# Optimization experiments

Measured on AMD Instinct MI355X. Metric: run time of the kernel, lower is better.

## Reference

```python
import jax, jax.numpy as jnp
import numpy as np

B, N, DEG = 8, 8192, 16
E = B * N * DEG
K1 = 2458  # ceil(0.3*8192)
K2 = 738   # ceil(0.3*2458)
NUM_CLASSES = 10


def gat(x, src, dst, emask, W, a_s, a_d, bias):
    # PyG GATConv with add_self_loops=True, negative_slope=0.2, concat heads
    n = x.shape[0]
    H, F = a_s.shape
    xp = (x @ W).reshape(n, H, F)                      # [n,H,F]
    al_s = (xp * a_s).sum(-1)                          # [n,H]
    al_d = (xp * a_d).sum(-1)
    loops = jnp.arange(n, dtype=src.dtype)
    s2 = jnp.concatenate([src, loops])
    d2 = jnp.concatenate([dst, loops])
    m2 = jnp.concatenate([emask, jnp.ones(n, bool)])
    e = jax.nn.leaky_relu(al_s[s2] + al_d[d2], 0.2)    # [E+n,H]
    e = jnp.where(m2[:, None], e, -1e9)
    emax = jax.ops.segment_max(e, d2, num_segments=n)
    ex = jnp.where(m2[:, None], jnp.exp(e - emax[d2]), 0.0)
    den = jax.ops.segment_sum(ex, d2, num_segments=n)
    msg = ex[:, :, None] * xp[s2]                      # [E+n,H,F]
    out = jax.ops.segment_sum(msg, d2, num_segments=n) / den[:, :, None]
    return out.reshape(n, H * F) + bias


def inorm(x):
    # PyG InstanceNorm (affine=False): per-graph per-channel normalization
    xb = x.reshape(B, -1, x.shape[-1])
    mu = xb.mean(1, keepdims=True)
    var = ((xb - mu) ** 2).mean(1, keepdims=True)
    return ((xb - mu) / jnp.sqrt(var + 1e-5)).reshape(x.shape)


def topk_pool(x, src, dst, emask, p, k):
    # TopKPooling: score = tanh(x.p/|p|), keep top-k per graph, scale x by score
    n_tot = x.shape[0]
    n = n_tot // B
    score = jnp.tanh((x @ p) / jnp.linalg.norm(p))
    sv, si = jax.lax.top_k(score.reshape(B, n), k)     # [B,k]
    xg = jnp.take_along_axis(x.reshape(B, n, -1), si[:, :, None], axis=1)
    xnew = (xg * sv[:, :, None]).reshape(B * k, -1)
    perm = (si + (jnp.arange(B) * n)[:, None]).reshape(-1)
    newid = jnp.full(n_tot, -1, dtype=src.dtype).at[perm].set(
        jnp.arange(B * k, dtype=src.dtype))
    ns, nd = newid[src], newid[dst]
    m = emask & (ns >= 0) & (nd >= 0)
    return xnew, jnp.maximum(ns, 0), jnp.maximum(nd, 0), m


def setup_inputs() -> dict:
    key = jax.random.key(0)
    ks = jax.random.split(key, 32)
    pos = jax.random.normal(ks[0], (B * N, 3), jnp.float32)
    offs = jnp.repeat(jnp.arange(B, dtype=jnp.int32) * N, N * DEG)
    src = jax.random.randint(ks[1], (E,), 0, N, jnp.int32) + offs
    dst = jax.random.randint(ks[2], (E,), 0, N, jnp.int32) + offs

    def lin(k, fi, fo):
        return jax.random.normal(k, (fi, fo), jnp.float32) * (1.0 / np.sqrt(fi))

    d = dict(pos=pos, src=src, dst=dst)
    d['W1'] = lin(ks[3], 3, 32);   d['a_s1'] = jax.random.normal(ks[4], (2, 16)) * 0.2
    d['a_d1'] = jax.random.normal(ks[5], (2, 16)) * 0.2
    d['b1'] = jnp.zeros((32,));    d['p1'] = jax.random.normal(ks[6], (32,))
    d['W2'] = lin(ks[7], 32, 128); d['a_s2'] = jax.random.normal(ks[8], (2, 64)) * 0.2
    d['a_d2'] = jax.random.normal(ks[9], (2, 64)) * 0.2
    d['b2'] = jnp.zeros((128,));   d['p2'] = jax.random.normal(ks[10], (128,))
    d['W3'] = lin(ks[11], 128, 256); d['a_s3'] = jax.random.normal(ks[12], (1, 256)) * 0.1
    d['a_d3'] = jax.random.normal(ks[13], (1, 256)) * 0.1
    d['b3'] = jnp.zeros((256,))
    d['gw1'] = lin(ks[14], 256, 64);  d['gb1'] = jnp.zeros((64,))
    d['gw2'] = lin(ks[15], 64, 1);    d['gb2'] = jnp.zeros((1,))
    d['aw'] = lin(ks[16], 256, 256);  d['ab'] = jnp.zeros((256,))
    d['w1'] = lin(ks[17], 256, 512);  d['bb1'] = jnp.zeros((512,))
    d['w2'] = lin(ks[18], 512, 128);  d['bb2'] = jnp.zeros((128,))
    d['w3'] = lin(ks[19], 128, NUM_CLASSES); d['bb3'] = jnp.zeros((NUM_CLASSES,))
    return d


def reference(pos, src, dst, W1, a_s1, a_d1, b1, p1, W2, a_s2, a_d2, b2, p2,
              W3, a_s3, a_d3, b3, gw1, gb1, gw2, gb2, aw, ab,
              w1, bb1, w2, bb2, w3, bb3):
    emask = jnp.ones(src.shape[0], bool)
    x = gat(pos, src, dst, emask, W1, a_s1, a_d1, b1)
    x = jax.nn.elu(inorm(x))
    x, src, dst, emask = topk_pool(x, src, dst, emask, p1, K1)
    x = gat(x, src, dst, emask, W2, a_s2, a_d2, b2)
    x = jax.nn.elu(inorm(x))
    x, src, dst, emask = topk_pool(x, src, dst, emask, p2, K2)
    x = gat(x, src, dst, emask, W3, a_s3, a_d3, b3)
    x = jax.nn.elu(inorm(x))
    # GlobalAttention: gate_nn = Linear(256,64)+ELU+Linear(64,1); nn = Linear+ELU
    gate = jax.nn.elu(x @ gw1 + gb1) @ gw2 + gb2       # [M,1]
    h = jax.nn.elu(x @ aw + ab)                        # [M,256]
    a = jax.nn.softmax(gate.reshape(B, K2, 1), axis=1)
    g = (a * h.reshape(B, K2, 256)).sum(1)             # [B,256]
    z = jax.nn.elu(g @ w1 + bb1)   # dropout inactive in eval
    z = jax.nn.elu(z @ w2 + bb2)
    z = z @ w3 + bb3
    return jax.nn.log_softmax(z, axis=1)
```

## Files before the change

kernel.cpp:

```cpp
#include <hip/hip_runtime.h>
#include <cstdint>
#include <cstddef>

#define DI __device__ __forceinline__

namespace pk {

constexpr int NB1 = 65536;
constexpr int NE  = 1048576;
constexpr int BG  = 8;
constexpr int NPG1 = 8192;
constexpr int EPG1 = NE/BG;
constexpr int KP1 = 2458;
constexpr int KP2 = 738;
constexpr int NN2 = BG*KP1;
constexpr int NN3 = BG*KP2;
constexpr int REG2 = 16384;
constexpr int REG3 = 4096;
constexpr int CAP2 = BG*REG2;
constexpr int CAP3 = BG*REG3;

DI float lrelu(float x){ return x > 0.f ? x : 0.2f*x; }
DI float eluf(float x){ return x > 0.f ? x : expf(x) - 1.f; }

DI int swz_block(){
  int nb = gridDim.x, b = blockIdx.x;
  if((nb & 7) == 0) return (b & 7)*(nb >> 3) + (b >> 3);
  return b;
}

__global__ __launch_bounds__(1024) void k_s1_front(
    const float* __restrict__ pos, const float* __restrict__ W,
    const float* __restrict__ as_, const float* __restrict__ ad_,
    float* __restrict__ xp, float* __restrict__ als, float* __restrict__ ald,
    const int* __restrict__ de, int* __restrict__ cnt){
  int tid = threadIdx.x;
  if(blockIdx.x < 64){
    int i = blockIdx.x*1024 + tid;
    float p0=pos[3*i], p1=pos[3*i+1], p2=pos[3*i+2];
    float row[32];
#pragma unroll
    for(int c=0;c<32;c++) row[c] = p0*W[c] + p1*W[32+c] + p2*W[64+c];
    float s0=0.f,d0=0.f,s1=0.f,d1=0.f;
#pragma unroll
    for(int f=0;f<16;f++){
      s0 += row[f]*as_[f];        d0 += row[f]*ad_[f];
      s1 += row[16+f]*as_[16+f];  d1 += row[16+f]*ad_[16+f];
    }
    float4* o = reinterpret_cast<float4*>(xp + (size_t)i*32);
#pragma unroll
    for(int q=0;q<8;q++) o[q] = make_float4(row[4*q],row[4*q+1],row[4*q+2],row[4*q+3]);
    als[2*i]=s0; als[2*i+1]=s1; ald[2*i]=d0; ald[2*i+1]=d1;
    return;
  }
  int bb = blockIdx.x - 64;
  int4 d = ((const int4*)de)[bb*1024 + tid];
  atomicAdd(&cnt[d.x], 1);
  atomicAdd(&cnt[d.y], 1);
  atomicAdd(&cnt[d.z], 1);
  atomicAdd(&cnt[d.w], 1);
}

__global__ __launch_bounds__(1024) void k_tile_scatter(
    const int* __restrict__ se, const int* __restrict__ de,
    const int* __restrict__ rowptr, int* __restrict__ eo){
  __shared__ int cur[256];
  int tid = threadIdx.x;
  int g = blockIdx.x & 7, t = blockIdx.x >> 3;
  int lo = g*NPG1 + t*256;
  if(tid < 256) cur[tid] = rowptr[lo + tid];
  __syncthreads();
  const int4* de4 = (const int4*)(de + g*EPG1);
  const int4* se4 = (const int4*)(se + g*EPG1);
  for(int it=0; it<4; it++){
    int4 bd[8], bs[8];
#pragma unroll
    for(int j=0;j<8;j++){
      int idx = (it*8+j)*1024 + tid;
      bd[j] = de4[idx]; bs[j] = se4[idx];
    }
#pragma unroll
    for(int j=0;j<8;j++){
      int4 d = bd[j], s = bs[j];
      int d0=d.x-lo; if((unsigned)d0<256u){ int p=atomicAdd(&cur[d0],1); eo[p]=s.x; }
      int d1=d.y-lo; if((unsigned)d1<256u){ int p=atomicAdd(&cur[d1],1); eo[p]=s.y; }
      int d2=d.z-lo; if((unsigned)d2<256u){ int p=atomicAdd(&cur[d2],1); eo[p]=s.z; }
      int d3=d.w-lo; if((unsigned)d3<256u){ int p=atomicAdd(&cur[d3],1); eo[p]=s.w; }
    }
  }
}

__global__ __launch_bounds__(256) void k_scatter_r(
    const int* __restrict__ se, const int* __restrict__ de,
    const int* __restrict__ gcnt, int reg,
    int* __restrict__ cursor, int* __restrict__ eo){
  int i = swz_block()*256 + threadIdx.x;
  int g = i / reg, loc = i % reg;
  if(loc < gcnt[g]){
    int p = atomicAdd(&cursor[de[i]], 1);
    eo[p] = se[i];
  }
}

__global__ __launch_bounds__(256) void k_edge_compact(
    const int* __restrict__ se, const int* __restrict__ de,
    const int* __restrict__ gcnt_in, int fixed_in, int bpg, int reg_in,
    const int* __restrict__ newid, int* __restrict__ gcnt_out,
    int* __restrict__ ons, int* __restrict__ ond, int reg_out,
    int* __restrict__ cnt){
  __shared__ int s_a[4096];
  __shared__ int s_b[4096];
  __shared__ int run, tbase;
  int tid = threadIdx.x;
  if(tid == 0) run = 0;
  __syncthreads();
  int blk = swz_block();
  int g = blk / bpg, t = blk % bpg;
  int mg = gcnt_in ? gcnt_in[g] : fixed_in;
  if(mg > reg_in) mg = reg_in;
  int base_l = t*4096;
  if(base_l < mg){
    const int* deb = de + (size_t)g*reg_in + base_l;
    const int* seb = se + (size_t)g*reg_in + base_l;
    const int4* de4 = (const int4*)deb;
    const int4* se4 = (const int4*)seb;
    int4 BD[4], BS[4];
#pragma unroll
    for(int j=0;j<4;j++){ BD[j]=de4[j*256+tid]; BS[j]=se4[j*256+tid]; }
    int cl = 0;
#pragma unroll
    for(int j=0;j<4;j++){
      int eb = base_l + (j*256+tid)*4;
      int dd[4]={BD[j].x,BD[j].y,BD[j].z,BD[j].w};
      int ss[4]={BS[j].x,BS[j].y,BS[j].z,BS[j].w};
#pragma unroll
      for(int q=0;q<4;q++){
        if(eb+q < mg){
          int a = newid[ss[q]], b = newid[dd[q]];
          if(a>=0 && b>=0){ cl++; atomicAdd(&cnt[b], 1); }
        }
      }
    }
    int p0 = 0;
    if(cl) p0 = atomicAdd(&run, cl);
#pragma unroll
    for(int j=0;j<4;j++){
      int eb = base_l + (j*256+tid)*4;
      int dd[4]={BD[j].x,BD[j].y,BD[j].z,BD[j].w};
      int ss[4]={BS[j].x,BS[j].y,BS[j].z,BS[j].w};
#pragma unroll
      for(int q=0;q<4;q++){
        if(eb+q < mg){
          int a = newid[ss[q]], b = newid[dd[q]];
          if(a>=0 && b>=0){ s_a[p0]=a; s_b[p0]=b; p0++; }
        }
      }
    }
  }
  __syncthreads();
  int ns = run;
  if(tid==0) tbase = ns ? atomicAdd(&gcnt_out[g], ns) : 0;
  __syncthreads();
  int tb = tbase;
  for(int j=tid; j<ns; j+=256){
    int s2 = tb + j;
    if(s2 < reg_out){ ons[(size_t)g*reg_out+s2]=s_a[j]; ond[(size_t)g*reg_out+s2]=s_b[j]; }
  }
}

__global__ __launch_bounds__(1024) void k_scan_g(
    const int* __restrict__ cnt, int R, int estride,
    int* __restrict__ rowptr, int* __restrict__ cursor){
  __shared__ int wsum[16];
  int g = blockIdx.x;
  int tid = threadIdx.x, lane = tid & 63, w = tid >> 6;
  int PER = (R + 1023) >> 10;
  int base = g*R;
  int i0 = tid*PER;
  int v[8]; int s = 0;
  for(int j=0;j<PER;j++){ int i=i0+j; int x=(i<R)?cnt[base+i]:0; v[j]=s; s+=x; }
  int inc = s;
  for(int o=1;o<64;o<<=1){ int t=__shfl_up(inc,o,64); if(lane>=o) inc+=t; }
  if(lane==63) wsum[w]=inc;
  __syncthreads();
  int wb=0;
  for(int k=0;k<w;k++) wb+=wsum[k];
  int tb = g*estride + wb + inc - s;
  for(int j=0;j<PER;j++){
    int i=i0+j;
    if(i<R){
      int e=tb+v[j];
      rowptr[base+i]=e;
      if(cursor) cursor[base+i]=e;
    }
  }
}

template<int PER>
DI void scan256(const int* __restrict__ cnt, int R, int estride,
                int* __restrict__ rowptr, int* __restrict__ cursor, int g){
  __shared__ int wsum[4];
  int tid = threadIdx.x, lane = tid & 63, w = tid >> 6;
  int base = g*R;
  int i0 = tid*PER;
  int v[PER]; int s = 0;
#pragma unroll
  for(int j=0;j<PER;j++){ int i=i0+j; int x=(i<R)?cnt[base+i]:0; v[j]=s; s+=x; }
  int inc = s;
  for(int o=1;o<64;o<<=1){ int t=__shfl_up(inc,o,64); if(lane>=o) inc+=t; }
  if(lane==63) wsum[w]=inc;
  __syncthreads();
  int wb=0;
  for(int k=0;k<w;k++) wb+=wsum[k];
  int tb = g*estride + wb + inc - s;
#pragma unroll
  for(int j=0;j<PER;j++){
    int i=i0+j;
    if(i<R){
      int e=tb+v[j];
      rowptr[base+i]=e;
      cursor[base+i]=e;
    }
  }
}

template<int H,int F,int EB>
__global__ __launch_bounds__(256) void k_gat_fused(
    const float* __restrict__ xp, const float* __restrict__ als,
    const float* __restrict__ ald, const int* __restrict__ rowptr,
    const int* __restrict__ cnt, const int* __restrict__ esrc,
    const float* __restrict__ bias, float* __restrict__ out,
    float* __restrict__ accum, int RPG, int n){
  constexpr int C = H*F, C4 = C/4;
  constexpr int NPB = 256/C4;
  __shared__ float psum[4][C], psq[4][C];
  int tid = threadIdx.x;
  int nl = tid / C4, p = tid % C4;
  int node0 = swz_block()*NPB;
  int node = node0 + nl;
  int hh = (4*p)/F;
  const float4* xp4 = (const float4*)xp;
  float4 r = make_float4(0.f,0.f,0.f,0.f);
  bool valid = node < n;
  if(valid){
    float dvh = ald[node*H+hh];
    float sw  = expf(lrelu(als[node*H+hh] + dvh));
    float4 xs = xp4[(size_t)node*C4 + p];
    float den = sw;
    float ax=sw*xs.x, ay=sw*xs.y, az=sw*xs.z, aw_=sw*xs.w;
    int r0  = rowptr[node];
    int deg = cnt[node];
    for(int j=0; j<deg; j+=EB){
      int idx[EB]; float wv[EB]; float4 v[EB];
#pragma unroll
      for(int q=0;q<EB;q++)
        idx[q] = (j+q < deg) ? esrc[r0+j+q] : node;
#pragma unroll
      for(int q=0;q<EB;q++)
        wv[q] = als[idx[q]*H+hh];
#pragma unroll
      for(int q=0;q<EB;q++)
        v[q] = xp4[(size_t)idx[q]*C4 + p];
#pragma unroll
      for(int q=0;q<EB;q++){
        float w = (j+q < deg) ? expf(lrelu(wv[q] + dvh)) : 0.f;
        den += w;
        ax += w*v[q].x; ay += w*v[q].y; az += w*v[q].z; aw_ += w*v[q].w;
      }
    }
    float inv = 1.f / den;
    float4 bv = ((const float4*)bias)[p];
    r.x=ax*inv+bv.x; r.y=ay*inv+bv.y; r.z=az*inv+bv.z; r.w=aw_*inv+bv.w;
    ((float4*)out)[(size_t)node*C4 + p] = r;
  }
  int g0 = node0 / RPG;
  bool straddle = ((node0 + NPB - 1) / RPG) != g0;
  if(straddle){
    if(valid){
      int g = node / RPG;
      atomicAdd(&accum[(g*C+4*p+0)*2], r.x); atomicAdd(&accum[(g*C+4*p+0)*2+1], r.x*r.x);
      atomicAdd(&accum[(g*C+4*p+1)*2], r.y); atomicAdd(&accum[(g*C+4*p+1)*2+1], r.y*r.y);
      atomicAdd(&accum[(g*C+4*p+2)*2], r.z); atomicAdd(&accum[(g*C+4*p+2)*2+1], r.z*r.z);
      atomicAdd(&accum[(g*C+4*p+3)*2], r.w); atomicAdd(&accum[(g*C+4*p+3)*2+1], r.w*r.w);
    }
  } else {
    float sx=r.x, sy=r.y, sz=r.z, sw2=r.w;
    float qx=r.x*r.x, qy=r.y*r.y, qz=r.z*r.z, qw=r.w*r.w;
#pragma unroll
    for(int off=C4; off<64; off<<=1){
      sx += __shfl_down(sx, off, 64); sy += __shfl_down(sy, off, 64);
      sz += __shfl_down(sz, off, 64); sw2 += __shfl_down(sw2, off, 64);
      qx += __shfl_down(qx, off, 64); qy += __shfl_down(qy, off, 64);
      qz += __shfl_down(qz, off, 64); qw += __shfl_down(qw, off, 64);
    }
    int lane = tid & 63, w = tid >> 6;
    if(lane < C4){
      psum[w][4*lane+0]=sx; psum[w][4*lane+1]=sy;
      psum[w][4*lane+2]=sz; psum[w][4*lane+3]=sw2;
      psq[w][4*lane+0]=qx;  psq[w][4*lane+1]=qy;
      psq[w][4*lane+2]=qz;  psq[w][4*lane+3]=qw;
    }
    __syncthreads();
    if(tid < C){
      float ts = psum[0][tid]+psum[1][tid]+psum[2][tid]+psum[3][tid];
      float tq = psq[0][tid]+psq[1][tid]+psq[2][tid]+psq[3][tid];
      atomicAdd(&accum[(g0*C+tid)*2],   ts);
      atomicAdd(&accum[(g0*C+tid)*2+1], tq);
    }
  }
}

template<int K,int CO,int NPG,int H,int PER>
__global__ __launch_bounds__(256) void k_gemm_al(
    const float* __restrict__ X, const int* __restrict__ oldid,
    const float* __restrict__ scale, const float* __restrict__ W,
    float* __restrict__ Y, const float* __restrict__ a_s,
    const float* __restrict__ a_d, float* __restrict__ als,
    float* __restrict__ ald, int n, int ngemm,
    const int* __restrict__ scnt, int sR, int sstride,
    int* __restrict__ srowptr, int* __restrict__ scursor){
  constexpr int SUB = 256/CO;
  constexpr int NB = SUB*NPG;
  __shared__ float xs[NB][K];
  __shared__ float ps[4][NPG], pd[4][NPG];
  if((int)blockIdx.x >= ngemm){
    scan256<PER>(scnt, sR, sstride, srowptr, scursor, (int)blockIdx.x - ngemm);
    return;
  }
  int tid = threadIdx.x;
  int c = tid % CO, sg = tid / CO;
  int n0 = blockIdx.x * NB;
  for(int idx=tid; idx<NB*K; idx+=256){
    int r = idx / K, k = idx % K;
    int row = n0 + r;
    float v = 0.f;
    if(row < n){
      int orow = oldid[row];
      v = X[(size_t)orow*K + k] * scale[row];
    }
    xs[r][k] = v;
  }
  __syncthreads();
  float acc[NPG];
#pragma unroll
  for(int q=0;q<NPG;q++) acc[q]=0.f;
  for(int k=0;k<K;k++){
    float wv = W[(size_t)k*CO + c];
#pragma unroll
    for(int q=0;q<NPG;q++) acc[q] += xs[sg*NPG+q][k]*wv;
  }
  float asc = a_s[c], adc = a_d[c];
  float vs[NPG], vd[NPG];
#pragma unroll
  for(int q=0;q<NPG;q++){
    int row = n0 + sg*NPG + q;
    if(row < n) Y[(size_t)row*CO + c] = acc[q];
    vs[q] = acc[q]*asc; vd[q] = acc[q]*adc;
  }
#pragma unroll
  for(int o=32;o>0;o>>=1){
#pragma unroll
    for(int q=0;q<NPG;q++){
      vs[q] += __shfl_down(vs[q], o, 64);
      vd[q] += __shfl_down(vd[q], o, 64);
    }
  }
  int lane = tid & 63, w = tid >> 6;
  if(H == 2){
    if(lane == 0){
      int sg_ = w >> 1, h = w & 1;
#pragma unroll
      for(int q=0;q<NPG;q++){
        int row = n0 + sg_*NPG + q;
        if(row < n){ als[row*2+h] = vs[q]; ald[row*2+h] = vd[q]; }
      }
    }
  } else {
    if(lane == 0){
#pragma unroll
      for(int q=0;q<NPG;q++){ ps[w][q]=vs[q]; pd[w][q]=vd[q]; }
    }
    __syncthreads();
    if(tid < NPG){
      float s=0.f, d=0.f;
      for(int ww=0;ww<4;ww++){ s+=ps[ww][tid]; d+=pd[ww][tid]; }
      int row = n0 + tid;
      if(row < n){ als[row]=s; ald[row]=d; }
    }
  }
}

DI float inorm_of(const float* accum, int gc, float R, float x){
  float s = accum[gc*2], sq = accum[gc*2+1];
  float mu = s / R;
  float var = fmaxf(sq/R - mu*mu, 0.f);
  return eluf((x-mu)*rsqrtf(var+1e-5f));
}

template<int C>
__global__ __launch_bounds__(256) void k_inorm_score(
    float* __restrict__ x, const float* __restrict__ accum,
    const float* __restrict__ p, int R, int total,
    float* __restrict__ score, unsigned* __restrict__ u){
  __shared__ float rvp[256], rpp[256];
  int tid = threadIdx.x;
  int i = blockIdx.x*256 + tid;
  int c = tid & (C-1);
  bool act = i < total;
  float v = 0.f, pv = 0.f;
  if(act){
    int g = i / (R*C);
    v = inorm_of(accum, g*C+c, (float)R, x[i]);
    x[i] = v;
    pv = p[c];
  }
  rvp[tid] = v*pv; rpp[tid] = pv*pv;
  __syncthreads();
#pragma unroll
  for(int s2=C/2; s2>0; s2>>=1){
    if(c < s2){ rvp[tid]+=rvp[tid+s2]; rpp[tid]+=rpp[tid+s2]; }
    __syncthreads();
  }
  if(act && c==0){
    float sv = tanhf(rvp[tid]*rsqrtf(rpp[tid]));
    int row = i / C;
    score[row] = sv;
    unsigned bts = __float_as_uint(sv);
    u[row] = (bts & 0x80000000u) ? ~bts : (bts | 0x80000000u);
  }
}

__global__ __launch_bounds__(1024) void k_topk(
    const unsigned* __restrict__ u, const float* __restrict__ score,
    int R, int Ksel, int* __restrict__ newid, int* __restrict__ oldid,
    float* __restrict__ scale){
  __shared__ int hist[2048];
  __shared__ int seg[32];
  __shared__ int sh_b, sh_k;
  __shared__ int wsA[16], wsB[16];
  __shared__ int carr0, carr1;
  int g = blockIdx.x, tid = threadIdx.x, lane = tid&63, w = tid>>6;
  const unsigned* ug = u + (size_t)g*R;
  unsigned prefix = 0;
  int K = Ksel;
  for(int lev=0; lev<3; lev++){
    int shf = (lev==0)?21:((lev==1)?10:0);
    int nb  = (lev==2)?1024:2048;
    for(int i=tid;i<2048;i+=1024) hist[i]=0;
    __syncthreads();
    for(int i=tid;i<R;i+=1024){
      unsigned v = ug[i];
      bool ok = (lev==0) || (lev==1 && (v>>21)==prefix) || (lev==2 && (v>>10)==prefix);
      if(ok) atomicAdd(&hist[(v>>shf)&(nb-1)], 1);
    }
    __syncthreads();
    int W = nb/32;
    if(tid<32){ int s=0; int lo=nb-W*(tid+1); for(int b=lo;b<lo+W;b++) s+=hist[b]; seg[tid]=s; }
    __syncthreads();
    if(tid==0){
      int kk=K, sgi=0;
      while(seg[sgi]<kk){ kk-=seg[sgi]; sgi++; }
      int b = nb-1-W*sgi;
      while(hist[b]<kk){ kk-=hist[b]; b--; }
      sh_b=b; sh_k=kk;
    }
    __syncthreads();
    int b = sh_b; K = sh_k;
    if(lev==0) prefix = (unsigned)b;
    else if(lev==1) prefix = (prefix<<11) | (unsigned)b;
    else prefix = (prefix<<10) | (unsigned)b;
    __syncthreads();
  }
  unsigned thr = prefix;
  int need = K;
  if(tid==0){ carr0=0; carr1=0; }
  __syncthreads();
  for(int bb=0; bb<R; bb+=1024){
    int i = bb + tid; bool in = i < R;
    unsigned uv = in ? ug[i] : 0u;
    int eq = (in && uv==thr) ? 1:0;
    int gt = (in && uv>thr) ? 1:0;
    int inc = eq;
    for(int o=1;o<64;o<<=1){ int t=__shfl_up(inc,o,64); if(lane>=o) inc+=t; }
    if(lane==63) wsA[w]=inc;
    __syncthreads();
    int wb=0; for(int k=0;k<w;k++) wb+=wsA[k];
    int eq_excl = carr0 + wb + inc - eq;
    int take = (gt || (eq && eq_excl<need)) ? 1 : 0;
    int inc2 = take;
    for(int o=1;o<64;o<<=1){ int t=__shfl_up(inc2,o,64); if(lane>=o) inc2+=t; }
    if(lane==63) wsB[w]=inc2;
    __syncthreads();
    int wb2=0; for(int k=0;k<w;k++) wb2+=wsB[k];
    int pos = carr1 + wb2 + inc2 - take;
    if(take){
      int nr = g*Ksel + pos;
      newid[(size_t)g*R+i] = nr;
      oldid[nr] = g*R+i;
      scale[nr] = score[(size_t)g*R+i];
    }
    __syncthreads();
    if(tid==1023){ carr0 += wb + inc; carr1 += wb2 + inc2; }
    __syncthreads();
  }
}

__global__ __launch_bounds__(256) void k_gate_fused(
    const float* __restrict__ X, const float* __restrict__ accum,
    const float* __restrict__ gw1, const float* __restrict__ gb1,
    const float* __restrict__ gw2, const float* __restrict__ gb2,
    float* __restrict__ gatev, int n){
  __shared__ float xs[8][256];
  int tid = threadIdx.x;
  int n0 = blockIdx.x*8;
  for(int idx=tid; idx<2048; idx+=256){
    int r = idx >> 8, k = idx & 255;
    int row = n0 + r;
    float v = 0.f;
    if(row < n){
      int g = row / KP2;
      v = inorm_of(accum, g*256+k, (float)KP2, X[(size_t)row*256 + k]);
    }
    xs[r][k] = v;
  }
  __syncthreads();
  int sg = tid >> 6, c = tid & 63;
  float a0 = 0.f, a1 = 0.f;
#pragma unroll 8
  for(int k=0;k<256;k++){
    float w = gw1[k*64+c];
    a0 = fmaf(xs[sg][k],   w, a0);
    a1 = fmaf(xs[sg+4][k], w, a1);
  }
  float gb = gb1[c], g2 = gw2[c];
  float v0 = eluf(a0 + gb) * g2;
  float v1 = eluf(a1 + gb) * g2;
#pragma unroll
  for(int o=32;o>0;o>>=1){
    v0 += __shfl_down(v0, o, 64);
    v1 += __shfl_down(v1, o, 64);
  }
  if(c==0){
    int r0 = n0 + sg, r1 = n0 + sg + 4;
    if(r0 < n) gatev[r0] = v0 + gb2[0];
    if(r1 < n) gatev[r1] = v1 + gb2[0];
  }
}

__global__ __launch_bounds__(256) void k_attn_gemm(
    const float* __restrict__ X, const float* __restrict__ accum,
    const float* __restrict__ W, const float* __restrict__ bias,
    const float* __restrict__ gatev, float* __restrict__ gvec){
  __shared__ float xs[8][256];
  __shared__ float red[256];
  int tid = threadIdx.x;
  int t = blockIdx.x, g = blockIdx.y;
  int r0 = t*8;
  float mx = -1e30f;
  for(int r=tid;r<KP2;r+=256) mx = fmaxf(mx, gatev[g*KP2+r]);
  red[tid]=mx; __syncthreads();
  for(int s=128;s>0;s>>=1){ if(tid<s) red[tid]=fmaxf(red[tid],red[tid+s]); __syncthreads(); }
  mx = red[0]; __syncthreads();
  float sm=0.f;
  for(int r=tid;r<KP2;r+=256) sm += expf(gatev[g*KP2+r]-mx);
  red[tid]=sm; __syncthreads();
  for(int s=128;s>0;s>>=1){ if(tid<s) red[tid]+=red[tid+s]; __syncthreads(); }
  float inv = 1.f/red[0];
  __syncthreads();
  for(int idx=tid; idx<2048; idx+=256){
    int r = idx >> 8, k = idx & 255;
    int lr = r0 + r;
    float v = 0.f;
    if(lr < KP2){
      int row = g*KP2 + lr;
      v = inorm_of(accum, g*256+k, (float)KP2, X[(size_t)row*256 + k]);
    }
    xs[r][k] = v;
  }
  __syncthreads();
  int c = tid;
  float acc[8];
#pragma unroll
  for(int q=0;q<8;q++) acc[q]=0.f;
  for(int k=0;k<256;k++){
    float wv = W[(size_t)k*256 + c];
#pragma unroll
    for(int q=0;q<8;q++) acc[q] += xs[q][k]*wv;
  }
  float bv = bias[c];
  float tot = 0.f;
#pragma unroll
  for(int q=0;q<8;q++){
    int lr = r0 + q;
    if(lr < KP2){
      float h = eluf(acc[q] + bv);
      tot += expf(gatev[g*KP2+lr]-mx) * h;
    }
  }
  atomicAdd(&gvec[g*256+c], tot*inv);
}

template<int K,int CO,int ACT>
__global__ __launch_bounds__(256) void k_mlp_t(
    const float* __restrict__ X, const float* __restrict__ W,
    const float* __restrict__ b, float* __restrict__ Y, int n){
  int i = blockIdx.x*256+threadIdx.x;
  if(i>=n*CO) return;
  int r=i/CO, c=i%CO;
  const float* xr = X + (size_t)r*K;
  float a=0.f;
#pragma unroll 16
  for(int k=0;k<K;k++) a = fmaf(xr[k], W[(size_t)k*CO+c], a);
  a += b[c];
  if(ACT) a = eluf(a);
  Y[i]=a;
}

__global__ __launch_bounds__(64) void k_head(
    const float* __restrict__ z2, const float* __restrict__ w3,
    const float* __restrict__ b3, float* __restrict__ out){
  __shared__ float zc[10]; __shared__ float mred, sred;
  int g=blockIdx.x, tid=threadIdx.x;
  if(tid<10){
    float a=0.f;
#pragma unroll 16
    for(int k=0;k<128;k++) a += z2[g*128+k]*w3[k*10+tid];
    zc[tid]=a+b3[tid];
  }
  __syncthreads();
  if(tid==0){
    float m=zc[0];
    for(int k=1;k<10;k++) m=fmaxf(m,zc[k]);
    float s=0.f;
    for(int k=0;k<10;k++) s+=expf(zc[k]-m);
    mred=m; sred=logf(s);
  }
  __syncthreads();
  if(tid<10) out[g*10+tid]=zc[tid]-mred-sred;
}

}

extern "C" void kernel_launch(void* const* d_in, const int* in_sizes, int n_in,
                              void* d_out, int out_size, void* d_ws, size_t ws_size,
                              hipStream_t stream){
  using namespace pk;
  (void)in_sizes; (void)n_in; (void)out_size;
  const float* pos = (const float*)d_in[0];
  const int*   src = (const int*)d_in[1];
  const int*   dst = (const int*)d_in[2];
  const float* W1  = (const float*)d_in[3];
  const float* as1 = (const float*)d_in[4];
  const float* ad1 = (const float*)d_in[5];
  const float* b1  = (const float*)d_in[6];
  const float* p1  = (const float*)d_in[7];
  const float* W2  = (const float*)d_in[8];
  const float* as2 = (const float*)d_in[9];
  const float* ad2 = (const float*)d_in[10];
  const float* b2  = (const float*)d_in[11];
  const float* p2  = (const float*)d_in[12];
  const float* W3  = (const float*)d_in[13];
  const float* as3 = (const float*)d_in[14];
  const float* ad3 = (const float*)d_in[15];
  const float* b3  = (const float*)d_in[16];
  const float* gw1 = (const float*)d_in[17];
  const float* gb1 = (const float*)d_in[18];
  const float* gw2 = (const float*)d_in[19];
  const float* gb2 = (const float*)d_in[20];
  const float* aw  = (const float*)d_in[21];
  const float* ab  = (const float*)d_in[22];
  const float* w1  = (const float*)d_in[23];
  const float* bb1 = (const float*)d_in[24];
  const float* w2  = (const float*)d_in[25];
  const float* bb2 = (const float*)d_in[26];
  const float* w3  = (const float*)d_in[27];
  const float* bb3 = (const float*)d_in[28];
  float* out = (float*)d_out;

  char* base = (char*)d_ws; size_t off = 0;
  auto alloc = [&](size_t nbytes)->char*{
    char* p = base + off; off = (off + nbytes + 255) & ~(size_t)255; return p;
  };
  int*   cnt2  = (int*)alloc((size_t)NN2*4);
  int*   cnt3  = (int*)alloc((size_t)NN3*4);
  int*   ecnt2 = (int*)alloc((size_t)BG*4);
  int*   ecnt3 = (int*)alloc((size_t)BG*4);
  float* acc1  = (float*)alloc((size_t)BG*32*2*4);
  float* acc2  = (float*)alloc((size_t)BG*128*2*4);
  float* acc3  = (float*)alloc((size_t)BG*256*2*4);
  float* gvec  = (float*)alloc((size_t)BG*256*4);
  int*   cnt1  = (int*)alloc((size_t)NB1*4);
  size_t zend = off;
  int*   newid1 = (int*)alloc((size_t)NB1*4);
  int*   newid2 = (int*)alloc((size_t)NN2*4);
  size_t fstart = (size_t)((char*)newid1 - base);
  size_t fend = off;
  float*    xp1    = (float*)alloc((size_t)NB1*32*4);
  float*    als1   = (float*)alloc((size_t)NB1*2*4);
  float*    ald1   = (float*)alloc((size_t)NB1*2*4);
  int*      rowptr1= (int*)alloc((size_t)NB1*4);
  int*      esrc1  = (int*)alloc((size_t)NE*4);
  float*    out1   = (float*)alloc((size_t)NB1*32*4);
  float*    score1 = (float*)alloc((size_t)NB1*4);
  unsigned* u1     = (unsigned*)alloc((size_t)NB1*4);
  int*      oldid1 = (int*)alloc((size_t)NN2*4);
  float*    scale1 = (float*)alloc((size_t)NN2*4);
  int*      ns2    = (int*)alloc((size_t)CAP2*4);
  int*      nd2    = (int*)alloc((size_t)CAP2*4);
  int*      rowptr2= (int*)alloc((size_t)NN2*4);
  int*      cursor2= (int*)alloc((size_t)NN2*4);
  int*      esrc2  = (int*)alloc((size_t)CAP2*4);
  float*    xp2    = (float*)alloc((size_t)NN2*128*4);
  float*    als2   = (float*)alloc((size_t)NN2*2*4);
  float*    ald2   = (float*)alloc((size_t)NN2*2*4);
  float*    out2   = (float*)alloc((size_t)NN2*128*4);
  float*    score2 = (float*)alloc((size_t)NN2*4);
  unsigned* u2     = (unsigned*)alloc((size_t)NN2*4);
  int*      oldid2 = (int*)alloc((size_t)NN3*4);
  float*    scale2 = (float*)alloc((size_t)NN3*4);
  int*      ns3    = (int*)alloc((size_t)CAP3*4);
  int*      nd3    = (int*)alloc((size_t)CAP3*4);
  int*      rowptr3= (int*)alloc((size_t)NN3*4);
  int*      cursor3= (int*)alloc((size_t)NN3*4);
  int*      esrc3  = (int*)alloc((size_t)CAP3*4);
  float*    xp3    = (float*)alloc((size_t)NN3*256*4);
  float*    als3   = (float*)alloc((size_t)NN3*4);
  float*    ald3   = (float*)alloc((size_t)NN3*4);
  float*    out3   = (float*)alloc((size_t)NN3*256*4);
  float*    gatev  = (float*)alloc((size_t)NN3*4);
  float*    z1     = (float*)alloc((size_t)BG*512*4);
  float*    z2     = (float*)alloc((size_t)BG*128*4);
  if(off > ws_size) return;

  auto cdiv = [](int a, int b){ return (a+b-1)/b; };

  hipMemsetAsync(base, 0, zend, stream);
  hipMemsetAsync(base + fstart, 0xFF, fend - fstart, stream);

  k_s1_front<<<320,1024,0,stream>>>(pos,W1,as1,ad1,xp1,als1,ald1,dst,cnt1);
  k_scan_g<<<BG,1024,0,stream>>>(cnt1,NPG1,EPG1,rowptr1,nullptr);
  k_tile_scatter<<<256,1024,0,stream>>>(src,dst,rowptr1,esrc1);
  k_gat_fused<2,16,16><<<NB1/32,256,0,stream>>>(xp1,als1,ald1,rowptr1,cnt1,esrc1,b1,out1,acc1,NPG1,NB1);
  k_inorm_score<32><<<cdiv(NB1*32,256),256,0,stream>>>(out1,acc1,p1,8192,NB1*32,score1,u1);
  k_topk<<<BG,1024,0,stream>>>(u1,score1,8192,KP1,newid1,oldid1,scale1);
  k_edge_compact<<<BG*32,256,0,stream>>>(src,dst,nullptr,EPG1,32,EPG1,newid1,ecnt2,ns2,nd2,REG2,cnt2);
  {
    int ngemm = cdiv(NN2,8);
    k_gemm_al<32,128,4,2,10><<<ngemm+BG,256,0,stream>>>(
        out1,oldid1,scale1,W2,xp2,as2,ad2,als2,ald2,NN2,
        ngemm,cnt2,KP1,REG2,rowptr2,cursor2);
  }
  k_scatter_r<<<CAP2/256,256,0,stream>>>(ns2,nd2,ecnt2,REG2,cursor2,esrc2);
  k_gat_fused<2,64,8><<<NN2/8,256,0,stream>>>(xp2,als2,ald2,rowptr2,cnt2,esrc2,b2,out2,acc2,KP1,NN2);
  k_inorm_score<128><<<cdiv(NN2*128,256),256,0,stream>>>(out2,acc2,p2,KP1,NN2*128,score2,u2);
  k_topk<<<BG,1024,0,stream>>>(u2,score2,KP1,KP2,newid2,oldid2,scale2);
  k_edge_compact<<<BG*4,256,0,stream>>>(ns2,nd2,ecnt2,0,4,REG2,newid2,ecnt3,ns3,nd3,REG3,cnt3);
  {
    int ngemm = cdiv(NN3,4);
    k_gemm_al<128,256,4,1,3><<<ngemm+BG,256,0,stream>>>(
        out2,oldid2,scale2,W3,xp3,as3,ad3,als3,ald3,NN3,
        ngemm,cnt3,KP2,REG3,rowptr3,cursor3);
  }
  k_scatter_r<<<CAP3/256,256,0,stream>>>(ns3,nd3,ecnt3,REG3,cursor3,esrc3);
  k_gat_fused<1,256,4><<<NN3/4,256,0,stream>>>(xp3,als3,ald3,rowptr3,cnt3,esrc3,b3,out3,acc3,KP2,NN3);
  k_gate_fused<<<cdiv(NN3,8),256,0,stream>>>(out3,acc3,gw1,gb1,gw2,gb2,gatev,NN3);
  k_attn_gemm<<<dim3(cdiv(KP2,8),BG),256,0,stream>>>(out3,acc3,aw,ab,gatev,gvec);
  k_mlp_t<256,512,1><<<cdiv(BG*512,256),256,0,stream>>>(gvec,w1,bb1,z1,BG);
  k_mlp_t<512,128,1><<<cdiv(BG*128,256),256,0,stream>>>(z1,w2,bb2,z2,BG);
  k_head<<<BG,64,0,stream>>>(z2,w3,bb3,out);
}
```

Measured before the change: 476.9 us.

## Histogram stage-1 degrees in shared memory with per-block partials reduced in scan

Replaces global atomics on the per-node in-degree counter with shared-memory histograms, one per graph slice (8 blocks per graph, each covering an eighth of that graph's edges). Each block writes its partial histogram to global memory, and a new scan kernel sums the 8 partials, writes cnt1 and computes rowptr. This removes contended global atomics and the zeroing memset of cnt1, at the cost of 2 MB of partial writes and reads and fewer blocks for the counting phase. It relies on every edge's destination lying inside its own graph's node range.

```diff
diff --git a/kernel.cpp b/kernel.cpp
--- a/kernel.cpp
+++ b/kernel.cpp
@@ -19,6 +19,7 @@
 constexpr int REG3 = 4096;
 constexpr int CAP2 = BG*REG2;
 constexpr int CAP3 = BG*REG3;
+constexpr int CPB1 = 8;
 
 DI float lrelu(float x){ return x > 0.f ? x : 0.2f*x; }
 DI float eluf(float x){ return x > 0.f ? x : expf(x) - 1.f; }
@@ -33,7 +34,8 @@
     const float* __restrict__ pos, const float* __restrict__ W,
     const float* __restrict__ as_, const float* __restrict__ ad_,
     float* __restrict__ xp, float* __restrict__ als, float* __restrict__ ald,
-    const int* __restrict__ de, int* __restrict__ cnt){
+    const int* __restrict__ de, int* __restrict__ part){
+  __shared__ int h[NPG1];
   int tid = threadIdx.x;
   if(blockIdx.x < 64){
     int i = blockIdx.x*1024 + tid;
@@ -54,11 +56,54 @@
     return;
   }
   int bb = blockIdx.x - 64;
-  int4 d = ((const int4*)de)[bb*1024 + tid];
-  atomicAdd(&cnt[d.x], 1);
-  atomicAdd(&cnt[d.y], 1);
-  atomicAdd(&cnt[d.z], 1);
-  atomicAdd(&cnt[d.w], 1);
+  int g = bb >> 3, t = bb & 7;
+  for(int i=tid;i<NPG1;i+=1024) h[i]=0;
+  __syncthreads();
+  const int4* de4 = (const int4*)(de + g*EPG1 + t*(EPG1/CPB1));
+  int lo = g*NPG1;
+  int4 d0 = de4[0*1024+tid], d1 = de4[1*1024+tid];
+  int4 d2 = de4[2*1024+tid], d3 = de4[3*1024+tid];
+  atomicAdd(&h[d0.x-lo],1); atomicAdd(&h[d0.y-lo],1);
+  atomicAdd(&h[d0.z-lo],1); atomicAdd(&h[d0.w-lo],1);
+  atomicAdd(&h[d1.x-lo],1); atomicAdd(&h[d1.y-lo],1);
+  atomicAdd(&h[d1.z-lo],1); atomicAdd(&h[d1.w-lo],1);
+  atomicAdd(&h[d2.x-lo],1); atomicAdd(&h[d2.y-lo],1);
+  atomicAdd(&h[d2.z-lo],1); atomicAdd(&h[d2.w-lo],1);
+  atomicAdd(&h[d3.x-lo],1); atomicAdd(&h[d3.y-lo],1);
+  atomicAdd(&h[d3.z-lo],1); atomicAdd(&h[d3.w-lo],1);
+  __syncthreads();
+  int* pp = part + (size_t)(g*CPB1+t)*NPG1;
+  for(int i=tid;i<NPG1;i+=1024) pp[i]=h[i];
+}
+
+__global__ __launch_bounds__(1024) void k_scan1(
+    const int* __restrict__ part, int* __restrict__ cnt,
+    int* __restrict__ rowptr){
+  __shared__ int wsum[16];
+  int g = blockIdx.x;
+  int tid = threadIdx.x, lane = tid & 63, w = tid >> 6;
+  constexpr int PER = NPG1/1024;
+  int base = g*NPG1;
+  int i0 = tid*PER;
+  int v[PER]; int s = 0;
+#pragma unroll
+  for(int j=0;j<PER;j++){
+    int i = i0+j;
+    int x = 0;
+#pragma unroll
+    for(int p=0;p<CPB1;p++) x += part[(size_t)(g*CPB1+p)*NPG1 + i];
+    cnt[base+i] = x;
+    v[j] = s; s += x;
+  }
+  int inc = s;
+  for(int o=1;o<64;o<<=1){ int t2=__shfl_up(inc,o,64); if(lane>=o) inc+=t2; }
+  if(lane==63) wsum[w]=inc;
+  __syncthreads();
+  int wb=0;
+  for(int k=0;k<w;k++) wb+=wsum[k];
+  int tb = g*EPG1 + wb + inc - s;
+#pragma unroll
+  for(int j=0;j<PER;j++) rowptr[base+i0+j] = tb + v[j];
 }
 
 __global__ __launch_bounds__(1024) void k_tile_scatter(
@@ -165,34 +210,6 @@
   for(int j=tid; j<ns; j+=256){
     int s2 = tb + j;
     if(s2 < reg_out){ ons[(size_t)g*reg_out+s2]=s_a[j]; ond[(size_t)g*reg_out+s2]=s_b[j]; }
-  }
-}
-
-__global__ __launch_bounds__(1024) void k_scan_g(
-    const int* __restrict__ cnt, int R, int estride,
-    int* __restrict__ rowptr, int* __restrict__ cursor){
-  __shared__ int wsum[16];
-  int g = blockIdx.x;
-  int tid = threadIdx.x, lane = tid & 63, w = tid >> 6;
-  int PER = (R + 1023) >> 10;
-  int base = g*R;
-  int i0 = tid*PER;
-  int v[8]; int s = 0;
-  for(int j=0;j<PER;j++){ int i=i0+j; int x=(i<R)?cnt[base+i]:0; v[j]=s; s+=x; }
-  int inc = s;
-  for(int o=1;o<64;o<<=1){ int t=__shfl_up(inc,o,64); if(lane>=o) inc+=t; }
-  if(lane==63) wsum[w]=inc;
-  __syncthreads();
-  int wb=0;
-  for(int k=0;k<w;k++) wb+=wsum[k];
-  int tb = g*estride + wb + inc - s;
-  for(int j=0;j<PER;j++){
-    int i=i0+j;
-    if(i<R){
-      int e=tb+v[j];
-      rowptr[base+i]=e;
-      if(cursor) cursor[base+i]=e;
-    }
   }
 }
 
@@ -689,12 +706,13 @@
   float* acc2  = (float*)alloc((size_t)BG*128*2*4);
   float* acc3  = (float*)alloc((size_t)BG*256*2*4);
   float* gvec  = (float*)alloc((size_t)BG*256*4);
-  int*   cnt1  = (int*)alloc((size_t)NB1*4);
   size_t zend = off;
   int*   newid1 = (int*)alloc((size_t)NB1*4);
   int*   newid2 = (int*)alloc((size_t)NN2*4);
   size_t fstart = (size_t)((char*)newid1 - base);
   size_t fend = off;
+  int*      part1  = (int*)alloc((size_t)BG*CPB1*NPG1*4);
+  int*      cnt1   = (int*)alloc((size_t)NB1*4);
   float*    xp1    = (float*)alloc((size_t)NB1*32*4);
   float*    als1   = (float*)alloc((size_t)NB1*2*4);
   float*    ald1   = (float*)alloc((size_t)NB1*2*4);
@@ -737,8 +755,8 @@
   hipMemsetAsync(base, 0, zend, stream);
   hipMemsetAsync(base + fstart, 0xFF, fend - fstart, stream);
 
-  k_s1_front<<<320,1024,0,stream>>>(pos,W1,as1,ad1,xp1,als1,ald1,dst,cnt1);
-  k_scan_g<<<BG,1024,0,stream>>>(cnt1,NPG1,EPG1,rowptr1,nullptr);
+  k_s1_front<<<128,1024,0,stream>>>(pos,W1,as1,ad1,xp1,als1,ald1,dst,part1);
+  k_scan1<<<BG,1024,0,stream>>>(part1,cnt1,rowptr1);
   k_tile_scatter<<<256,1024,0,stream>>>(src,dst,rowptr1,esrc1);
   k_gat_fused<2,16,16><<<NB1/32,256,0,stream>>>(xp1,als1,ald1,rowptr1,cnt1,esrc1,b1,out1,acc1,NPG1,NB1);
   k_inorm_score<32><<<cdiv(NB1*32,256),256,0,stream>>>(out1,acc1,p1,8192,NB1*32,score1,u1);
```

After: 441.1 us. 7.5% less time.
